# Kernel optimization log

Hardware: AMD Instinct MI355X
Metric: run time of the kernel (lower is better)

Reference implementation:

```python
import jax, jax.numpy as jnp
import numpy as np

B = 1024          # number of graphs
H = 8             # heads
EPS = 1e-5        # LayerNorm eps (torch default)
MEAN_RES_SCALE = 0.2


def _ln(x, w, b):
    mu = x.mean(-1, keepdims=True)
    var = ((x - mu) ** 2).mean(-1, keepdims=True)
    return (x - mu) / jnp.sqrt(var + EPS) * w + b


def setup_inputs() -> dict:
    key = jax.random.key(0)
    ks = jax.random.split(key, 10)
    N, D = 262144, 256
    s = 1.0 / np.sqrt(D)
    return {
        "h": jax.random.normal(ks[0], (N, D), jnp.float32),
        "batch": jnp.sort(jax.random.randint(ks[1], (N,), 0, B)),
        "cdr_mask": jax.random.bernoulli(ks[2], 0.2, (N,)),
        "iface_mask": jax.random.bernoulli(ks[3], 0.2, (N,)),
        "ln_kv_w": jnp.ones((D,), jnp.float32),
        "ln_kv_b": jnp.zeros((D,), jnp.float32),
        "ln_q_w": jnp.ones((D,), jnp.float32),
        "ln_q_b": jnp.zeros((D,), jnp.float32),
        "Wk": jax.random.normal(ks[4], (D, D), jnp.float32) * s,
        "Wv": jax.random.normal(ks[5], (D, D), jnp.float32) * s,
        "Wq": jax.random.normal(ks[6], (D, 2 * D), jnp.float32) * (1.0 / np.sqrt(2 * D)),
        "Wres": jax.random.normal(ks[7], (D, D), jnp.float32) * s,
        "Wout": jax.random.normal(ks[8], (D, D), jnp.float32) * s,
        "cdr_bias": jnp.asarray(0.6, jnp.float32),
        "iface_bias": jnp.asarray(0.8, jnp.float32),
        "logit_scale": jnp.asarray(1.0, jnp.float32),
    }


def reference(h, batch, cdr_mask, iface_mask, ln_kv_w, ln_kv_b, ln_q_w, ln_q_b,
              Wk, Wv, Wq, Wres, Wout, cdr_bias, iface_bias, logit_scale):
    N, D = h.shape
    hd = D // H
    # per-graph mean / max pooling (segment reductions; all segments non-empty)
    counts = jax.ops.segment_sum(jnp.ones((N,), h.dtype), batch, num_segments=B)[:, None]
    mean_raw = jax.ops.segment_sum(h, batch, num_segments=B) / counts      # [B,D]
    max_raw = jax.ops.segment_max(h, batch, num_segments=B)                # [B,D]
    # single query per graph (dropout = identity in eval)
    q = jnp.concatenate([mean_raw, max_raw], axis=-1) @ Wq.T               # [B,D]
    q = _ln(q, ln_q_w, ln_q_b).reshape(B, H, hd)                           # [B,H,hd]
    # keys / values per node
    h_ln = _ln(h, ln_kv_w, ln_kv_b)
    k = (h_ln @ Wk.T).reshape(N, H, hd)
    v = (h_ln @ Wv.T).reshape(N, H, hd)
    # attention logits with mask biases
    logit = (k * q[batch]).sum(-1) * (logit_scale / np.sqrt(hd))           # [N,H]
    logit = logit + cdr_bias * cdr_mask.astype(h.dtype)[:, None]
    logit = logit + iface_bias * iface_mask.astype(h.dtype)[:, None]
    # segment softmax over nodes of each graph
    m = jax.ops.segment_max(logit, batch, num_segments=B)                  # [B,H]
    e = jnp.exp(logit - m[batch])
    z = jax.ops.segment_sum(e, batch, num_segments=B)                      # [B,H]
    attn = e / z[batch]                                                    # [N,H]
    g = jax.ops.segment_sum(attn[..., None] * v, batch, num_segments=B)    # [B,H,hd]
    g = g.reshape(B, D)
    return g @ Wout.T + MEAN_RES_SCALE * (mean_raw @ Wres.T)               # [B,D]
```

## Files before the change

### kernel.cpp

```cpp
#include <hip/hip_runtime.h>

__global__ void k_offsets(const int* __restrict__ batch, const int* __restrict__ cdr,
                          const int* __restrict__ ifm, const float* __restrict__ cdr_bias,
                          const float* __restrict__ iface_bias,
                          int* __restrict__ start, float* __restrict__ mbias,
                          int N, int B) {
    int i = blockIdx.x * blockDim.x + threadIdx.x;
    if (i >= N) return;
    mbias[i] = cdr_bias[0] * (float)cdr[i] + iface_bias[0] * (float)ifm[i];
    int b = batch[i];
    if (i == 0) {
        for (int g = 0; g <= b; ++g) start[g] = 0;
    } else {
        int pb = batch[i - 1];
        for (int g = pb + 1; g <= b; ++g) start[g] = i;
    }
    if (i == N - 1) {
        for (int g = b + 1; g <= B; ++g) start[g] = N;
    }
}

__global__ __launch_bounds__(256) void k_pool(
    const float* __restrict__ h, const int* __restrict__ start,
    float* __restrict__ psum, float* __restrict__ pmax, float2* __restrict__ stat)
{
    const int g = blockIdx.x >> 2;
    const int sl = blockIdx.x & 3;
    const int tid = threadIdx.x;
    const int w = tid >> 6;
    const int l = tid & 63;
    const int s = start[g], e = start[g + 1];
    const int len = e - s;
    const int qs = s + (len * sl) / 4;
    const int qe = s + (len * (sl + 1)) / 4;

    float4 sm = make_float4(0.f, 0.f, 0.f, 0.f);
    float4 mx = make_float4(-INFINITY, -INFINITY, -INFINITY, -INFINITY);

    #define PROC(v, rowidx) do { \
        sm.x += (v).x; sm.y += (v).y; sm.z += (v).z; sm.w += (v).w; \
        mx.x = fmaxf(mx.x, (v).x); mx.y = fmaxf(mx.y, (v).y); \
        mx.z = fmaxf(mx.z, (v).z); mx.w = fmaxf(mx.w, (v).w); \
        float s1_ = ((v).x + (v).y) + ((v).z + (v).w); \
        float s2_ = fmaf((v).x, (v).x, fmaf((v).y, (v).y, fmaf((v).z, (v).z, (v).w * (v).w))); \
        s1_ += __shfl_xor(s1_, 1);  s2_ += __shfl_xor(s2_, 1); \
        s1_ += __shfl_xor(s1_, 2);  s2_ += __shfl_xor(s2_, 2); \
        s1_ += __shfl_xor(s1_, 4);  s2_ += __shfl_xor(s2_, 4); \
        s1_ += __shfl_xor(s1_, 8);  s2_ += __shfl_xor(s2_, 8); \
        s1_ += __shfl_xor(s1_, 16); s2_ += __shfl_xor(s2_, 16); \
        s1_ += __shfl_xor(s1_, 32); s2_ += __shfl_xor(s2_, 32); \
        if (l == 0) { \
            const float mu_ = s1_ * (1.f / 256.f); \
            const float var_ = s2_ * (1.f / 256.f) - mu_ * mu_; \
            stat[rowidx] = make_float2(mu_, rsqrtf(var_ + 1e-5f)); \
        } } while (0)

    int n = qs + w;
    if (n + 12 < qe) {
        float4 f0 = *(const float4*)(h + (size_t)(n)      * 256 + l * 4);
        float4 f1 = *(const float4*)(h + (size_t)(n + 4)  * 256 + l * 4);
        float4 f2 = *(const float4*)(h + (size_t)(n + 8)  * 256 + l * 4);
        float4 f3 = *(const float4*)(h + (size_t)(n + 12) * 256 + l * 4);
        for (; n + 28 < qe; n += 16) {
            PROC(f0, n);      f0 = *(const float4*)(h + (size_t)(n + 16) * 256 + l * 4);
            PROC(f1, n + 4);  f1 = *(const float4*)(h + (size_t)(n + 20) * 256 + l * 4);
            PROC(f2, n + 8);  f2 = *(const float4*)(h + (size_t)(n + 24) * 256 + l * 4);
            PROC(f3, n + 12); f3 = *(const float4*)(h + (size_t)(n + 28) * 256 + l * 4);
        }
        PROC(f0, n); PROC(f1, n + 4); PROC(f2, n + 8); PROC(f3, n + 12);
        n += 16;
    }
    for (; n < qe; n += 4) {
        const float4 a = *(const float4*)(h + (size_t)n * 256 + l * 4);
        PROC(a, n);
    }
    #undef PROC

    __shared__ __align__(16) float PS[4][256];
    __shared__ __align__(16) float PM[4][256];
    *(float4*)(&PS[w][l * 4]) = sm;
    *(float4*)(&PM[w][l * 4]) = mx;
    __syncthreads();
    const int d = tid;
    const float sum = (PS[0][d] + PS[1][d]) + (PS[2][d] + PS[3][d]);
    const float mxv = fmaxf(fmaxf(PM[0][d], PM[1][d]), fmaxf(PM[2][d], PM[3][d]));
    psum[(size_t)blockIdx.x * 256 + d] = sum;
    pmax[(size_t)blockIdx.x * 256 + d] = mxv;
}

__global__ __launch_bounds__(256) void k_q(
    const float* __restrict__ psum, const float* __restrict__ pmax,
    const int* __restrict__ start,
    const float* __restrict__ Wq, const float* __restrict__ Wk,
    const float* __restrict__ ln_q_w, const float* __restrict__ ln_q_b,
    const float* __restrict__ ln_kv_w, const float* __restrict__ logit_scale,
    float* __restrict__ mean_raw, float* __restrict__ w_eff)
{
    const int g = blockIdx.x;
    const int d = threadIdx.x;
    const int s = start[g], e = start[g + 1];

    float sum = 0.f, mxv = -INFINITY;
    #pragma unroll
    for (int sl = 0; sl < 4; ++sl) {
        sum += psum[((size_t)g * 4 + sl) * 256 + d];
        mxv = fmaxf(mxv, pmax[((size_t)g * 4 + sl) * 256 + d]);
    }
    const float mean = sum / (float)(e - s);
    mean_raw[(size_t)g * 256 + d] = mean;

    __shared__ __align__(16) float X[512];
    __shared__ float QL[256];
    __shared__ float rs[4], rq[4];
    X[d] = mean;
    X[256 + d] = mxv;
    __syncthreads();

    float q = 0.f;
    const float* wqr = Wq + (size_t)d * 512;
    #pragma unroll 8
    for (int j = 0; j < 512; j += 4) {
        float4 w4 = *(const float4*)(wqr + j);
        q += w4.x * X[j] + w4.y * X[j + 1] + w4.z * X[j + 2] + w4.w * X[j + 3];
    }
    float s1 = q, s2 = q * q;
    #pragma unroll
    for (int off = 1; off < 64; off <<= 1) {
        s1 += __shfl_xor(s1, off);
        s2 += __shfl_xor(s2, off);
    }
    if ((d & 63) == 0) { rs[d >> 6] = s1; rq[d >> 6] = s2; }
    __syncthreads();
    const float t1 = rs[0] + rs[1] + rs[2] + rs[3];
    const float t2 = rq[0] + rq[1] + rq[2] + rq[3];
    const float mu = t1 * (1.f / 256.f);
    const float var = t2 * (1.f / 256.f) - mu * mu;
    const float rstd = rsqrtf(var + 1e-5f);
    QL[d] = (q - mu) * rstd * ln_q_w[d] + ln_q_b[d];
    __syncthreads();

    const float scale = logit_scale[0] * 0.17677669529663687f;
    const float fold = scale * ln_kv_w[d];
    #pragma unroll
    for (int hh = 0; hh < 8; ++hh) {
        float a = 0.f;
        #pragma unroll 8
        for (int r = 0; r < 32; ++r) {
            a += Wk[(size_t)(hh * 32 + r) * 256 + d] * QL[hh * 32 + r];
        }
        w_eff[((size_t)g * 8 + hh) * 256 + d] = a * fold;
    }
}

__global__ __launch_bounds__(256) void k_attn(
    const float* __restrict__ h, const int* __restrict__ start,
    const float* __restrict__ mbias, const float2* __restrict__ stat,
    const float* __restrict__ ln_w, const float* __restrict__ ln_b,
    const float* __restrict__ w_eff,
    float* __restrict__ u_norm)
{
    const int g = blockIdx.x;
    const int tid = threadIdx.x;
    const int w = tid >> 6;
    const int l = tid & 63;
    const int hh = l >> 3;
    const int p = l & 7;
    const int s = start[g], e = start[g + 1];

    float we[32];
    {
        const float* wp = w_eff + ((size_t)g * 8 + hh) * 256 + p * 32;
        #pragma unroll
        for (int r = 0; r < 8; ++r) {
            float4 t = *(const float4*)(wp + r * 4);
            we[4 * r + 0] = t.x; we[4 * r + 1] = t.y; we[4 * r + 2] = t.z; we[4 * r + 3] = t.w;
        }
    }
    float s1h = 0.f;
    #pragma unroll
    for (int r = 0; r < 32; ++r) s1h += we[r];
    s1h += __shfl_xor(s1h, 1);
    s1h += __shfl_xor(s1h, 2);
    s1h += __shfl_xor(s1h, 4);

    float m = -INFINITY, z = 0.f, sw = 0.f;
    float u[32];
    #pragma unroll
    for (int r = 0; r < 32; ++r) u[r] = 0.f;

    __shared__ __align__(16) float hbuf[4][288];
    __shared__ __align__(16) float UF[4][8][264];
    __shared__ float MW[4][8], ZW[4][8], SW[4][8], FG[4][8], IZ[8], SG[8];

    const int wofs = l * 4 + ((l >> 3) << 2);
    const int rofs = p * 36;

    int n = s + w;
    float4 x0 = make_float4(0.f, 0.f, 0.f, 0.f);
    float4 x1 = x0;
    float b0 = 0.f, b1 = 0.f;
    float2 t0 = make_float2(0.f, 1.f), t1 = t0;
    if (n < e)     { x0 = *(const float4*)(h + (size_t)n * 256 + l * 4);
                     b0 = mbias[n];     t0 = stat[n]; }
    if (n + 4 < e) { x1 = *(const float4*)(h + (size_t)(n + 4) * 256 + l * 4);
                     b1 = mbias[n + 4]; t1 = stat[n + 4]; }

    while (n < e) {
        const float4 xc = x0;
        const float bc = b0;
        const float2 tc = t0;
        x0 = x1; b0 = b1; t0 = t1;
        if (n + 8 < e) {
            x1 = *(const float4*)(h + (size_t)(n + 8) * 256 + l * 4);
            b1 = mbias[n + 8];
            t1 = stat[n + 8];
        }

        *(float4*)(&hbuf[w][wofs]) = xc;
        asm volatile("s_waitcnt lgkmcnt(0)" ::: "memory");

        float hv[32];
        #pragma unroll
        for (int r = 0; r < 8; ++r) {
            float4 t = *(const float4*)(&hbuf[w][rofs + r * 4]);
            hv[4 * r + 0] = t.x; hv[4 * r + 1] = t.y; hv[4 * r + 2] = t.z; hv[4 * r + 3] = t.w;
        }
        float d0 = 0.f, d1 = 0.f, d2 = 0.f, d3 = 0.f;
        #pragma unroll
        for (int r = 0; r < 8; ++r) {
            d0 = fmaf(hv[4 * r + 0], we[4 * r + 0], d0);
            d1 = fmaf(hv[4 * r + 1], we[4 * r + 1], d1);
            d2 = fmaf(hv[4 * r + 2], we[4 * r + 2], d2);
            d3 = fmaf(hv[4 * r + 3], we[4 * r + 3], d3);
        }
        float dt = (d0 + d1) + (d2 + d3);
        dt += __shfl_xor(dt, 1);
        dt += __shfl_xor(dt, 2);
        dt += __shfl_xor(dt, 4);

        const float mu = tc.x, rstd = tc.y;
        const float lv = fmaf(rstd, dt - mu * s1h, bc);

        const float nm = fmaxf(m, lv);
        const float ee = __expf(lv - nm);
        const float c = ee * rstd;
        if (__any(lv > m)) {
            const float a = __expf(m - nm);
            z = z * a + ee;
            sw = sw * a + c * mu;
            #pragma unroll
            for (int r = 0; r < 32; ++r) u[r] = u[r] * a + c * hv[r];
            m = nm;
        } else {
            z += ee;
            sw += c * mu;
            #pragma unroll
            for (int r = 0; r < 32; ++r) u[r] = fmaf(c, hv[r], u[r]);
        }
        n += 4;
    }

    if (p == 0) { MW[w][hh] = m; ZW[w][hh] = z; SW[w][hh] = sw; }
    #pragma unroll
    for (int r = 0; r < 8; ++r) {
        float4 t = make_float4(u[4 * r], u[4 * r + 1], u[4 * r + 2], u[4 * r + 3]);
        *(float4*)(&UF[w][hh][p * 32 + r * 4]) = t;
    }
    __syncthreads();

    if (tid < 8) {
        const float mg = fmaxf(fmaxf(MW[0][tid], MW[1][tid]),
                               fmaxf(MW[2][tid], MW[3][tid]));
        float zg = 0.f, sg = 0.f;
        #pragma unroll
        for (int ww = 0; ww < 4; ++ww) {
            const float f = __expf(MW[ww][tid] - mg);
            FG[ww][tid] = f;
            zg += ZW[ww][tid] * f;
            sg += SW[ww][tid] * f;
        }
        IZ[tid] = 1.f / zg;
        SG[tid] = sg;
    }
    __syncthreads();

    const float lwj = ln_w[tid], lbj = ln_b[tid];
    #pragma unroll
    for (int h2 = 0; h2 < 8; ++h2) {
        const float Uv = UF[0][h2][tid] * FG[0][h2] + UF[1][h2][tid] * FG[1][h2]
                       + UF[2][h2][tid] * FG[2][h2] + UF[3][h2][tid] * FG[3][h2];
        u_norm[(size_t)g * 2048 + h2 * 256 + tid] = (Uv - SG[h2]) * IZ[h2] * lwj + lbj;
    }
}

__global__ __launch_bounds__(256) void k_out(
    const float* __restrict__ u_norm, const float* __restrict__ mean_raw,
    const float* __restrict__ Wv, const float* __restrict__ Wout,
    const float* __restrict__ Wres, float* __restrict__ out)
{
    const int d = threadIdx.x;
    const int g = blockIdx.x;
    __shared__ __align__(16) float UN[8][256];
    __shared__ __align__(16) float MR[256];
    __shared__ __align__(16) float GF[256];

    const float4* up = (const float4*)(u_norm + (size_t)g * 2048);
    ((float4*)UN)[d] = up[d];
    ((float4*)UN)[256 + d] = up[256 + d];
    if (d < 64) ((float4*)MR)[d] = ((const float4*)(mean_raw + (size_t)g * 256))[d];
    __syncthreads();

    const int hh = d >> 5;
    float acc = 0.f;
    const float* wvr = Wv + (size_t)d * 256;
    #pragma unroll 8
    for (int j = 0; j < 256; j += 4) {
        const float4 wv = *(const float4*)(wvr + j);
        const float4 uv = *(const float4*)(&UN[hh][j]);
        acc += wv.x * uv.x + wv.y * uv.y + wv.z * uv.z + wv.w * uv.w;
    }
    GF[d] = acc;
    __syncthreads();

    float oo = 0.f, rr = 0.f;
    const float* wor = Wout + (size_t)d * 256;
    const float* wrr = Wres + (size_t)d * 256;
    #pragma unroll 8
    for (int j = 0; j < 256; j += 4) {
        const float4 wo = *(const float4*)(wor + j);
        const float4 wq = *(const float4*)(wrr + j);
        const float4 gf = *(const float4*)(&GF[j]);
        const float4 mr = *(const float4*)(&MR[j]);
        oo += wo.x * gf.x + wo.y * gf.y + wo.z * gf.z + wo.w * gf.w;
        rr += wq.x * mr.x + wq.y * mr.y + wq.z * mr.z + wq.w * mr.w;
    }
    out[(size_t)g * 256 + d] = oo + 0.2f * rr;
}

extern "C" void kernel_launch(void* const* d_in, const int* in_sizes, int n_in,
                              void* d_out, int out_size, void* d_ws, size_t ws_size,
                              hipStream_t stream)
{
    const float* h        = (const float*)d_in[0];
    const int*   batch    = (const int*)d_in[1];
    const int*   cdr      = (const int*)d_in[2];
    const int*   ifm      = (const int*)d_in[3];
    const float* ln_kv_w  = (const float*)d_in[4];
    const float* ln_kv_b  = (const float*)d_in[5];
    const float* ln_q_w   = (const float*)d_in[6];
    const float* ln_q_b   = (const float*)d_in[7];
    const float* Wk       = (const float*)d_in[8];
    const float* Wv       = (const float*)d_in[9];
    const float* Wq       = (const float*)d_in[10];
    const float* Wres     = (const float*)d_in[11];
    const float* Wout     = (const float*)d_in[12];
    const float* cdr_b    = (const float*)d_in[13];
    const float* if_b     = (const float*)d_in[14];
    const float* lsc      = (const float*)d_in[15];

    const int N = in_sizes[0] / 256;
    const int B = out_size / 256;

    int*    start    = (int*)d_ws;
    float*  mean_raw = (float*)((char*)d_ws + 8192);
    float*  w_eff    = mean_raw + (size_t)B * 256;
    float*  u_norm   = w_eff + (size_t)B * 2048;
    float*  psum     = u_norm + (size_t)B * 2048;
    float*  pmax     = psum + (size_t)B * 1024;
    float*  mbias    = pmax + (size_t)B * 1024;
    float2* stat     = (float2*)(mbias + (size_t)N);

    k_offsets<<<(N + 255) / 256, 256, 0, stream>>>(batch, cdr, ifm, cdr_b, if_b,
                                                   start, mbias, N, B);
    k_pool<<<B * 4, 256, 0, stream>>>(h, start, psum, pmax, stat);
    k_q<<<B, 256, 0, stream>>>(psum, pmax, start, Wq, Wk, ln_q_w, ln_q_b, ln_kv_w,
                               lsc, mean_raw, w_eff);
    k_attn<<<B, 256, 0, stream>>>(h, start, mbias, stat, ln_kv_w, ln_kv_b, w_eff, u_norm);
    k_out<<<B, 256, 0, stream>>>(u_norm, mean_raw, Wv, Wout, Wres, (float*)d_out);
}
```

Before: 652.8 us.

## Fuse pooling, query, attention and output into one per-graph kernel

Merges the pool, query, attention and output kernels into a single kernel with one block per graph, so intermediates (pooled sums/max, w_eff, u_norm, per-row LayerNorm stats) stay in shared memory instead of round-tripping through global memory. Per-row stats are cached in LDS up to a fixed cap and recomputed with wave reductions beyond it. The pooling pass now runs with B blocks instead of 4B, cutting parallelism for the h read. The second h pass may hit cache sooner because the same block rereads its own rows right after pooling.

Result: faster. 619.7 us (-5.1%).

```diff
diff --git a/kernel.cpp b/kernel.cpp
--- a/kernel.cpp
+++ b/kernel.cpp
@@ -20,144 +20,18 @@
     }
 }
 
-__global__ __launch_bounds__(256) void k_pool(
+#define STAT_CAP 768
+
+__global__ __launch_bounds__(256) void k_fused(
     const float* __restrict__ h, const int* __restrict__ start,
-    float* __restrict__ psum, float* __restrict__ pmax, float2* __restrict__ stat)
-{
-    const int g = blockIdx.x >> 2;
-    const int sl = blockIdx.x & 3;
-    const int tid = threadIdx.x;
-    const int w = tid >> 6;
-    const int l = tid & 63;
-    const int s = start[g], e = start[g + 1];
-    const int len = e - s;
-    const int qs = s + (len * sl) / 4;
-    const int qe = s + (len * (sl + 1)) / 4;
-
-    float4 sm = make_float4(0.f, 0.f, 0.f, 0.f);
-    float4 mx = make_float4(-INFINITY, -INFINITY, -INFINITY, -INFINITY);
-
-    #define PROC(v, rowidx) do { \
-        sm.x += (v).x; sm.y += (v).y; sm.z += (v).z; sm.w += (v).w; \
-        mx.x = fmaxf(mx.x, (v).x); mx.y = fmaxf(mx.y, (v).y); \
-        mx.z = fmaxf(mx.z, (v).z); mx.w = fmaxf(mx.w, (v).w); \
-        float s1_ = ((v).x + (v).y) + ((v).z + (v).w); \
-        float s2_ = fmaf((v).x, (v).x, fmaf((v).y, (v).y, fmaf((v).z, (v).z, (v).w * (v).w))); \
-        s1_ += __shfl_xor(s1_, 1);  s2_ += __shfl_xor(s2_, 1); \
-        s1_ += __shfl_xor(s1_, 2);  s2_ += __shfl_xor(s2_, 2); \
-        s1_ += __shfl_xor(s1_, 4);  s2_ += __shfl_xor(s2_, 4); \
-        s1_ += __shfl_xor(s1_, 8);  s2_ += __shfl_xor(s2_, 8); \
-        s1_ += __shfl_xor(s1_, 16); s2_ += __shfl_xor(s2_, 16); \
-        s1_ += __shfl_xor(s1_, 32); s2_ += __shfl_xor(s2_, 32); \
-        if (l == 0) { \
-            const float mu_ = s1_ * (1.f / 256.f); \
-            const float var_ = s2_ * (1.f / 256.f) - mu_ * mu_; \
-            stat[rowidx] = make_float2(mu_, rsqrtf(var_ + 1e-5f)); \
-        } } while (0)
-
-    int n = qs + w;
-    if (n + 12 < qe) {
-        float4 f0 = *(const float4*)(h + (size_t)(n)      * 256 + l * 4);
-        float4 f1 = *(const float4*)(h + (size_t)(n + 4)  * 256 + l * 4);
-        float4 f2 = *(const float4*)(h + (size_t)(n + 8)  * 256 + l * 4);
-        float4 f3 = *(const float4*)(h + (size_t)(n + 12) * 256 + l * 4);
-        for (; n + 28 < qe; n += 16) {
-            PROC(f0, n);      f0 = *(const float4*)(h + (size_t)(n + 16) * 256 + l * 4);
-            PROC(f1, n + 4);  f1 = *(const float4*)(h + (size_t)(n + 20) * 256 + l * 4);
-            PROC(f2, n + 8);  f2 = *(const float4*)(h + (size_t)(n + 24) * 256 + l * 4);
-            PROC(f3, n + 12); f3 = *(const float4*)(h + (size_t)(n + 28) * 256 + l * 4);
-        }
-        PROC(f0, n); PROC(f1, n + 4); PROC(f2, n + 8); PROC(f3, n + 12);
-        n += 16;
-    }
-    for (; n < qe; n += 4) {
-        const float4 a = *(const float4*)(h + (size_t)n * 256 + l * 4);
-        PROC(a, n);
-    }
-    #undef PROC
-
-    __shared__ __align__(16) float PS[4][256];
-    __shared__ __align__(16) float PM[4][256];
-    *(float4*)(&PS[w][l * 4]) = sm;
-    *(float4*)(&PM[w][l * 4]) = mx;
-    __syncthreads();
-    const int d = tid;
-    const float sum = (PS[0][d] + PS[1][d]) + (PS[2][d] + PS[3][d]);
-    const float mxv = fmaxf(fmaxf(PM[0][d], PM[1][d]), fmaxf(PM[2][d], PM[3][d]));
-    psum[(size_t)blockIdx.x * 256 + d] = sum;
-    pmax[(size_t)blockIdx.x * 256 + d] = mxv;
-}
-
-__global__ __launch_bounds__(256) void k_q(
-    const float* __restrict__ psum, const float* __restrict__ pmax,
-    const int* __restrict__ start,
+    const float* __restrict__ mbias,
+    const float* __restrict__ lnkw, const float* __restrict__ lnkb,
     const float* __restrict__ Wq, const float* __restrict__ Wk,
     const float* __restrict__ ln_q_w, const float* __restrict__ ln_q_b,
-    const float* __restrict__ ln_kv_w, const float* __restrict__ logit_scale,
-    float* __restrict__ mean_raw, float* __restrict__ w_eff)
-{
-    const int g = blockIdx.x;
-    const int d = threadIdx.x;
-    const int s = start[g], e = start[g + 1];
-
-    float sum = 0.f, mxv = -INFINITY;
-    #pragma unroll
-    for (int sl = 0; sl < 4; ++sl) {
-        sum += psum[((size_t)g * 4 + sl) * 256 + d];
-        mxv = fmaxf(mxv, pmax[((size_t)g * 4 + sl) * 256 + d]);
-    }
-    const float mean = sum / (float)(e - s);
-    mean_raw[(size_t)g * 256 + d] = mean;
-
-    __shared__ __align__(16) float X[512];
-    __shared__ float QL[256];
-    __shared__ float rs[4], rq[4];
-    X[d] = mean;
-    X[256 + d] = mxv;
-    __syncthreads();
-
-    float q = 0.f;
-    const float* wqr = Wq + (size_t)d * 512;
-    #pragma unroll 8
-    for (int j = 0; j < 512; j += 4) {
-        float4 w4 = *(const float4*)(wqr + j);
-        q += w4.x * X[j] + w4.y * X[j + 1] + w4.z * X[j + 2] + w4.w * X[j + 3];
-    }
-    float s1 = q, s2 = q * q;
-    #pragma unroll
-    for (int off = 1; off < 64; off <<= 1) {
-        s1 += __shfl_xor(s1, off);
-        s2 += __shfl_xor(s2, off);
-    }
-    if ((d & 63) == 0) { rs[d >> 6] = s1; rq[d >> 6] = s2; }
-    __syncthreads();
-    const float t1 = rs[0] + rs[1] + rs[2] + rs[3];
-    const float t2 = rq[0] + rq[1] + rq[2] + rq[3];
-    const float mu = t1 * (1.f / 256.f);
-    const float var = t2 * (1.f / 256.f) - mu * mu;
-    const float rstd = rsqrtf(var + 1e-5f);
-    QL[d] = (q - mu) * rstd * ln_q_w[d] + ln_q_b[d];
-    __syncthreads();
-
-    const float scale = logit_scale[0] * 0.17677669529663687f;
-    const float fold = scale * ln_kv_w[d];
-    #pragma unroll
-    for (int hh = 0; hh < 8; ++hh) {
-        float a = 0.f;
-        #pragma unroll 8
-        for (int r = 0; r < 32; ++r) {
-            a += Wk[(size_t)(hh * 32 + r) * 256 + d] * QL[hh * 32 + r];
-        }
-        w_eff[((size_t)g * 8 + hh) * 256 + d] = a * fold;
-    }
-}
-
-__global__ __launch_bounds__(256) void k_attn(
-    const float* __restrict__ h, const int* __restrict__ start,
-    const float* __restrict__ mbias, const float2* __restrict__ stat,
-    const float* __restrict__ ln_w, const float* __restrict__ ln_b,
-    const float* __restrict__ w_eff,
-    float* __restrict__ u_norm)
+    const float* __restrict__ logit_scale,
+    const float* __restrict__ Wv, const float* __restrict__ Wout,
+    const float* __restrict__ Wres,
+    float* __restrict__ out)
 {
     const int g = blockIdx.x;
     const int tid = threadIdx.x;
@@ -166,15 +40,125 @@
     const int hh = l >> 3;
     const int p = l & 7;
     const int s = start[g], e = start[g + 1];
+    const int len = e - s;
+
+    __shared__ __align__(16) float SMEM[8448];
+    __shared__ __align__(16) float hbuf[4][288];
+    __shared__ __align__(16) float MR[256];
+    __shared__ float MW[4][8], ZW[4][8], SW[4][8], FG[4][8], IZ[8], SG[8];
+    __shared__ float rs[4], rq[4];
+
+    float* const PS  = SMEM;
+    float* const PM  = SMEM + 1024;
+    float* const X   = SMEM;
+    float* const QL  = SMEM + 512;
+    float* const WE  = SMEM + 768;
+    float* const STT = SMEM + 2880;
+
+    {
+        float4 sm = make_float4(0.f, 0.f, 0.f, 0.f);
+        float4 mx = make_float4(-INFINITY, -INFINITY, -INFINITY, -INFINITY);
+
+        #define PROC(v, rowidx) do { \
+            sm.x += (v).x; sm.y += (v).y; sm.z += (v).z; sm.w += (v).w; \
+            mx.x = fmaxf(mx.x, (v).x); mx.y = fmaxf(mx.y, (v).y); \
+            mx.z = fmaxf(mx.z, (v).z); mx.w = fmaxf(mx.w, (v).w); \
+            float s1_ = ((v).x + (v).y) + ((v).z + (v).w); \
+            float s2_ = fmaf((v).x, (v).x, fmaf((v).y, (v).y, fmaf((v).z, (v).z, (v).w * (v).w))); \
+            s1_ += __shfl_xor(s1_, 1);  s2_ += __shfl_xor(s2_, 1); \
+            s1_ += __shfl_xor(s1_, 2);  s2_ += __shfl_xor(s2_, 2); \
+            s1_ += __shfl_xor(s1_, 4);  s2_ += __shfl_xor(s2_, 4); \
+            s1_ += __shfl_xor(s1_, 8);  s2_ += __shfl_xor(s2_, 8); \
+            s1_ += __shfl_xor(s1_, 16); s2_ += __shfl_xor(s2_, 16); \
+            s1_ += __shfl_xor(s1_, 32); s2_ += __shfl_xor(s2_, 32); \
+            const int ri_ = (rowidx) - s; \
+            if (l == 0 && ri_ < STAT_CAP) { \
+                const float mu_ = s1_ * (1.f / 256.f); \
+                const float var_ = s2_ * (1.f / 256.f) - mu_ * mu_; \
+                *(float2*)(&STT[2 * ri_]) = make_float2(mu_, rsqrtf(var_ + 1e-5f)); \
+            } } while (0)
+
+        int n = s + w;
+        if (n + 12 < e) {
+            float4 f0 = *(const float4*)(h + (size_t)(n)      * 256 + l * 4);
+            float4 f1 = *(const float4*)(h + (size_t)(n + 4)  * 256 + l * 4);
+            float4 f2 = *(const float4*)(h + (size_t)(n + 8)  * 256 + l * 4);
+            float4 f3 = *(const float4*)(h + (size_t)(n + 12) * 256 + l * 4);
+            for (; n + 28 < e; n += 16) {
+                PROC(f0, n);      f0 = *(const float4*)(h + (size_t)(n + 16) * 256 + l * 4);
+                PROC(f1, n + 4);  f1 = *(const float4*)(h + (size_t)(n + 20) * 256 + l * 4);
+                PROC(f2, n + 8);  f2 = *(const float4*)(h + (size_t)(n + 24) * 256 + l * 4);
+                PROC(f3, n + 12); f3 = *(const float4*)(h + (size_t)(n + 28) * 256 + l * 4);
+            }
+            PROC(f0, n); PROC(f1, n + 4); PROC(f2, n + 8); PROC(f3, n + 12);
+            n += 16;
+        }
+        for (; n < e; n += 4) {
+            const float4 a = *(const float4*)(h + (size_t)n * 256 + l * 4);
+            PROC(a, n);
+        }
+        #undef PROC
+
+        *(float4*)(&PS[w * 256 + l * 4]) = sm;
+        *(float4*)(&PM[w * 256 + l * 4]) = mx;
+    }
+    __syncthreads();
+
+    const int d = tid;
+    {
+        const float sum = (PS[d] + PS[256 + d]) + (PS[512 + d] + PS[768 + d]);
+        const float mxv = fmaxf(fmaxf(PM[d], PM[256 + d]),
+                                fmaxf(PM[512 + d], PM[768 + d]));
+        const float mean = sum / (float)len;
+        MR[d] = mean;
+        X[d] = mean;
+        X[256 + d] = mxv;
+    }
+    __syncthreads();
+
+    {
+        float q = 0.f;
+        const float* wqr = Wq + (size_t)d * 512;
+        #pragma unroll 8
+        for (int j = 0; j < 512; j += 4) {
+            float4 w4 = *(const float4*)(wqr + j);
+            q += w4.x * X[j] + w4.y * X[j + 1] + w4.z * X[j + 2] + w4.w * X[j + 3];
+        }
+        float s1 = q, s2 = q * q;
+        #pragma unroll
+        for (int off = 1; off < 64; off <<= 1) {
+            s1 += __shfl_xor(s1, off);
+            s2 += __shfl_xor(s2, off);
+        }
+        if ((d & 63) == 0) { rs[d >> 6] = s1; rq[d >> 6] = s2; }
+        __syncthreads();
+        const float t1 = rs[0] + rs[1] + rs[2] + rs[3];
+        const float t2 = rq[0] + rq[1] + rq[2] + rq[3];
+        const float mu = t1 * (1.f / 256.f);
+        const float var = t2 * (1.f / 256.f) - mu * mu;
+        const float rstd = rsqrtf(var + 1e-5f);
+        QL[d] = (q - mu) * rstd * ln_q_w[d] + ln_q_b[d];
+        __syncthreads();
+
+        const float scale = logit_scale[0] * 0.17677669529663687f;
+        const float fold = scale * lnkw[d];
+        #pragma unroll
+        for (int h2 = 0; h2 < 8; ++h2) {
+            float a = 0.f;
+            #pragma unroll 8
+            for (int r = 0; r < 32; ++r) {
+                a += Wk[(size_t)(h2 * 32 + r) * 256 + d] * QL[h2 * 32 + r];
+            }
+            WE[h2 * 264 + d] = a * fold;
+        }
+    }
+    __syncthreads();
 
     float we[32];
-    {
-        const float* wp = w_eff + ((size_t)g * 8 + hh) * 256 + p * 32;
-        #pragma unroll
-        for (int r = 0; r < 8; ++r) {
-            float4 t = *(const float4*)(wp + r * 4);
-            we[4 * r + 0] = t.x; we[4 * r + 1] = t.y; we[4 * r + 2] = t.z; we[4 * r + 3] = t.w;
-        }
+    #pragma unroll
+    for (int r = 0; r < 8; ++r) {
+        float4 t = *(const float4*)(&WE[hh * 264 + p * 32 + r * 4]);
+        we[4 * r + 0] = t.x; we[4 * r + 1] = t.y; we[4 * r + 2] = t.z; we[4 * r + 3] = t.w;
     }
     float s1h = 0.f;
     #pragma unroll
@@ -188,83 +172,92 @@
     #pragma unroll
     for (int r = 0; r < 32; ++r) u[r] = 0.f;
 
-    __shared__ __align__(16) float hbuf[4][288];
-    __shared__ __align__(16) float UF[4][8][264];
-    __shared__ float MW[4][8], ZW[4][8], SW[4][8], FG[4][8], IZ[8], SG[8];
-
     const int wofs = l * 4 + ((l >> 3) << 2);
     const int rofs = p * 36;
 
-    int n = s + w;
-    float4 x0 = make_float4(0.f, 0.f, 0.f, 0.f);
-    float4 x1 = x0;
-    float b0 = 0.f, b1 = 0.f;
-    float2 t0 = make_float2(0.f, 1.f), t1 = t0;
-    if (n < e)     { x0 = *(const float4*)(h + (size_t)n * 256 + l * 4);
-                     b0 = mbias[n];     t0 = stat[n]; }
-    if (n + 4 < e) { x1 = *(const float4*)(h + (size_t)(n + 4) * 256 + l * 4);
-                     b1 = mbias[n + 4]; t1 = stat[n + 4]; }
-
-    while (n < e) {
-        const float4 xc = x0;
-        const float bc = b0;
-        const float2 tc = t0;
-        x0 = x1; b0 = b1; t0 = t1;
-        if (n + 8 < e) {
-            x1 = *(const float4*)(h + (size_t)(n + 8) * 256 + l * 4);
-            b1 = mbias[n + 8];
-            t1 = stat[n + 8];
-        }
-
-        *(float4*)(&hbuf[w][wofs]) = xc;
-        asm volatile("s_waitcnt lgkmcnt(0)" ::: "memory");
-
-        float hv[32];
-        #pragma unroll
-        for (int r = 0; r < 8; ++r) {
-            float4 t = *(const float4*)(&hbuf[w][rofs + r * 4]);
-            hv[4 * r + 0] = t.x; hv[4 * r + 1] = t.y; hv[4 * r + 2] = t.z; hv[4 * r + 3] = t.w;
-        }
-        float d0 = 0.f, d1 = 0.f, d2 = 0.f, d3 = 0.f;
-        #pragma unroll
-        for (int r = 0; r < 8; ++r) {
-            d0 = fmaf(hv[4 * r + 0], we[4 * r + 0], d0);
-            d1 = fmaf(hv[4 * r + 1], we[4 * r + 1], d1);
-            d2 = fmaf(hv[4 * r + 2], we[4 * r + 2], d2);
-            d3 = fmaf(hv[4 * r + 3], we[4 * r + 3], d3);
-        }
-        float dt = (d0 + d1) + (d2 + d3);
-        dt += __shfl_xor(dt, 1);
-        dt += __shfl_xor(dt, 2);
-        dt += __shfl_xor(dt, 4);
-
-        const float mu = tc.x, rstd = tc.y;
-        const float lv = fmaf(rstd, dt - mu * s1h, bc);
-
-        const float nm = fmaxf(m, lv);
-        const float ee = __expf(lv - nm);
-        const float c = ee * rstd;
-        if (__any(lv > m)) {
-            const float a = __expf(m - nm);
-            z = z * a + ee;
-            sw = sw * a + c * mu;
+    {
+        int n = s + w;
+        float4 x0 = make_float4(0.f, 0.f, 0.f, 0.f);
+        float4 x1 = x0;
+        float b0 = 0.f, b1 = 0.f;
+        if (n < e)     { x0 = *(const float4*)(h + (size_t)n * 256 + l * 4);       b0 = mbias[n]; }
+        if (n + 4 < e) { x1 = *(const float4*)(h + (size_t)(n + 4) * 256 + l * 4); b1 = mbias[n + 4]; }
+
+        while (n < e) {
+            const float4 xc = x0;
+            const float bc = b0;
+            x0 = x1; b0 = b1;
+            if (n + 8 < e) {
+                x1 = *(const float4*)(h + (size_t)(n + 8) * 256 + l * 4);
+                b1 = mbias[n + 8];
+            }
+
+            float mu, rstd;
+            const int ri = n - s;
+            if (ri < STAT_CAP) {
+                const float2 tc = *(const float2*)(&STT[2 * ri]);
+                mu = tc.x; rstd = tc.y;
+            } else {
+                float s1 = (xc.x + xc.y) + (xc.z + xc.w);
+                float s2 = fmaf(xc.x, xc.x, fmaf(xc.y, xc.y, fmaf(xc.z, xc.z, xc.w * xc.w)));
+                #pragma unroll
+                for (int off = 1; off < 64; off <<= 1) {
+                    s1 += __shfl_xor(s1, off);
+                    s2 += __shfl_xor(s2, off);
+                }
+                mu = s1 * (1.f / 256.f);
+                rstd = rsqrtf(s2 * (1.f / 256.f) - mu * mu + 1e-5f);
+            }
+
+            *(float4*)(&hbuf[w][wofs]) = xc;
+            asm volatile("s_waitcnt lgkmcnt(0)" ::: "memory");
+
+            float hv[32];
             #pragma unroll
-            for (int r = 0; r < 32; ++r) u[r] = u[r] * a + c * hv[r];
-            m = nm;
-        } else {
-            z += ee;
-            sw += c * mu;
+            for (int r = 0; r < 8; ++r) {
+                float4 t = *(const float4*)(&hbuf[w][rofs + r * 4]);
+                hv[4 * r + 0] = t.x; hv[4 * r + 1] = t.y; hv[4 * r + 2] = t.z; hv[4 * r + 3] = t.w;
+            }
+            float d0 = 0.f, d1 = 0.f, d2 = 0.f, d3 = 0.f;
             #pragma unroll
-            for (int r = 0; r < 32; ++r) u[r] = fmaf(c, hv[r], u[r]);
-        }
-        n += 4;
-    }
-
+            for (int r = 0; r < 8; ++r) {
+                d0 = fmaf(hv[4 * r + 0], we[4 * r + 0], d0);
+                d1 = fmaf(hv[4 * r + 1], we[4 * r + 1], d1);
+                d2 = fmaf(hv[4 * r + 2], we[4 * r + 2], d2);
+                d3 = fmaf(hv[4 * r + 3], we[4 * r + 3], d3);
+            }
+            float dt = (d0 + d1) + (d2 + d3);
+            dt += __shfl_xor(dt, 1);
+            dt += __shfl_xor(dt, 2);
+            dt += __shfl_xor(dt, 4);
+
+            const float lv = fmaf(rstd, dt - mu * s1h, bc);
+            const float nm = fmaxf(m, lv);
+            const float ee = __expf(lv - nm);
+            const float c = ee * rstd;
+            if (__any(lv > m)) {
+                const float a = __expf(m - nm);
+                z = z * a + ee;
+                sw = sw * a + c * mu;
+                #pragma unroll
+                for (int r = 0; r < 32; ++r) u[r] = u[r] * a + c * hv[r];
+                m = nm;
+            } else {
+                z += ee;
+                sw += c * mu;
+                #pragma unroll
+                for (int r = 0; r < 32; ++r) u[r] = fmaf(c, hv[r], u[r]);
+            }
+            n += 4;
+        }
+    }
+
+    __syncthreads();
     if (p == 0) { MW[w][hh] = m; ZW[w][hh] = z; SW[w][hh] = sw; }
     #pragma unroll
     for (int r = 0; r < 8; ++r) {
         float4 t = make_float4(u[4 * r], u[4 * r + 1], u[4 * r + 2], u[4 * r + 3]);
-        *(float4*)(&UF[w][hh][p * 32 + r * 4]) = t;
+        *(float4*)(&SMEM[w * 2112 + hh * 264 + p * 32 + r * 4]) = t;
     }
     __syncthreads();
 
@@ -284,57 +277,51 @@
     }
     __syncthreads();
 
-    const float lwj = ln_w[tid], lbj = ln_b[tid];
-    #pragma unroll
-    for (int h2 = 0; h2 < 8; ++h2) {
-        const float Uv = UF[0][h2][tid] * FG[0][h2] + UF[1][h2][tid] * FG[1][h2]
-                       + UF[2][h2][tid] * FG[2][h2] + UF[3][h2][tid] * FG[3][h2];
-        u_norm[(size_t)g * 2048 + h2 * 256 + tid] = (Uv - SG[h2]) * IZ[h2] * lwj + lbj;
-    }
-}
-
-__global__ __launch_bounds__(256) void k_out(
-    const float* __restrict__ u_norm, const float* __restrict__ mean_raw,
-    const float* __restrict__ Wv, const float* __restrict__ Wout,
-    const float* __restrict__ Wres, float* __restrict__ out)
-{
-    const int d = threadIdx.x;
-    const int g = blockIdx.x;
-    __shared__ __align__(16) float UN[8][256];
-    __shared__ __align__(16) float MR[256];
-    __shared__ __align__(16) float GF[256];
-
-    const float4* up = (const float4*)(u_norm + (size_t)g * 2048);
-    ((float4*)UN)[d] = up[d];
-    ((float4*)UN)[256 + d] = up[256 + d];
-    if (d < 64) ((float4*)MR)[d] = ((const float4*)(mean_raw + (size_t)g * 256))[d];
-    __syncthreads();
-
-    const int hh = d >> 5;
-    float acc = 0.f;
-    const float* wvr = Wv + (size_t)d * 256;
-    #pragma unroll 8
-    for (int j = 0; j < 256; j += 4) {
-        const float4 wv = *(const float4*)(wvr + j);
-        const float4 uv = *(const float4*)(&UN[hh][j]);
-        acc += wv.x * uv.x + wv.y * uv.y + wv.z * uv.z + wv.w * uv.w;
-    }
-    GF[d] = acc;
-    __syncthreads();
-
-    float oo = 0.f, rr = 0.f;
-    const float* wor = Wout + (size_t)d * 256;
-    const float* wrr = Wres + (size_t)d * 256;
-    #pragma unroll 8
-    for (int j = 0; j < 256; j += 4) {
-        const float4 wo = *(const float4*)(wor + j);
-        const float4 wq = *(const float4*)(wrr + j);
-        const float4 gf = *(const float4*)(&GF[j]);
-        const float4 mr = *(const float4*)(&MR[j]);
-        oo += wo.x * gf.x + wo.y * gf.y + wo.z * gf.z + wo.w * gf.w;
-        rr += wq.x * mr.x + wq.y * mr.y + wq.z * mr.z + wq.w * mr.w;
-    }
-    out[(size_t)g * 256 + d] = oo + 0.2f * rr;
+    float un[8];
+    {
+        const float lwj = lnkw[tid], lbj = lnkb[tid];
+        #pragma unroll
+        for (int h2 = 0; h2 < 8; ++h2) {
+            const float Uv = SMEM[0 * 2112 + h2 * 264 + tid] * FG[0][h2]
+                           + SMEM[1 * 2112 + h2 * 264 + tid] * FG[1][h2]
+                           + SMEM[2 * 2112 + h2 * 264 + tid] * FG[2][h2]
+                           + SMEM[3 * 2112 + h2 * 264 + tid] * FG[3][h2];
+            un[h2] = (Uv - SG[h2]) * IZ[h2] * lwj + lbj;
+        }
+    }
+    __syncthreads();
+    #pragma unroll
+    for (int h2 = 0; h2 < 8; ++h2) SMEM[h2 * 256 + tid] = un[h2];
+    __syncthreads();
+
+    {
+        const int h5 = d >> 5;
+        float acc = 0.f;
+        const float* wvr = Wv + (size_t)d * 256;
+        #pragma unroll 8
+        for (int j = 0; j < 256; j += 4) {
+            const float4 wv = *(const float4*)(wvr + j);
+            const float4 uv = *(const float4*)(&SMEM[h5 * 256 + j]);
+            acc += wv.x * uv.x + wv.y * uv.y + wv.z * uv.z + wv.w * uv.w;
+        }
+        SMEM[2048 + d] = acc;
+    }
+    __syncthreads();
+    {
+        float oo = 0.f, rr = 0.f;
+        const float* wor = Wout + (size_t)d * 256;
+        const float* wrr = Wres + (size_t)d * 256;
+        #pragma unroll 8
+        for (int j = 0; j < 256; j += 4) {
+            const float4 wo = *(const float4*)(wor + j);
+            const float4 wq = *(const float4*)(wrr + j);
+            const float4 gf = *(const float4*)(&SMEM[2048 + j]);
+            const float4 mr = *(const float4*)(&MR[j]);
+            oo += wo.x * gf.x + wo.y * gf.y + wo.z * gf.z + wo.w * gf.w;
+            rr += wq.x * mr.x + wq.y * mr.y + wq.z * mr.z + wq.w * mr.w;
+        }
+        out[(size_t)g * 256 + d] = oo + 0.2f * rr;
+    }
 }
 
 extern "C" void kernel_launch(void* const* d_in, const int* in_sizes, int n_in,
@@ -361,20 +348,12 @@
     const int N = in_sizes[0] / 256;
     const int B = out_size / 256;
 
-    int*    start    = (int*)d_ws;
-    float*  mean_raw = (float*)((char*)d_ws + 8192);
-    float*  w_eff    = mean_raw + (size_t)B * 256;
-    float*  u_norm   = w_eff + (size_t)B * 2048;
-    float*  psum     = u_norm + (size_t)B * 2048;
-    float*  pmax     = psum + (size_t)B * 1024;
-    float*  mbias    = pmax + (size_t)B * 1024;
-    float2* stat     = (float2*)(mbias + (size_t)N);
+    int*   start = (int*)d_ws;
+    float* mbias = (float*)((char*)d_ws + 8192);
 
     k_offsets<<<(N + 255) / 256, 256, 0, stream>>>(batch, cdr, ifm, cdr_b, if_b,
                                                    start, mbias, N, B);
-    k_pool<<<B * 4, 256, 0, stream>>>(h, start, psum, pmax, stat);
-    k_q<<<B, 256, 0, stream>>>(psum, pmax, start, Wq, Wk, ln_q_w, ln_q_b, ln_kv_w,
-                               lsc, mean_raw, w_eff);
-    k_attn<<<B, 256, 0, stream>>>(h, start, mbias, stat, ln_kv_w, ln_kv_b, w_eff, u_norm);
-    k_out<<<B, 256, 0, stream>>>(u_norm, mean_raw, Wv, Wout, Wres, (float*)d_out);
+    k_fused<<<B, 256, 0, stream>>>(h, start, mbias, ln_kv_w, ln_kv_b,
+                                   Wq, Wk, ln_q_w, ln_q_b, lsc,
+                                   Wv, Wout, Wres, (float*)d_out);
 }
```
